# Kernel optimization log

Hardware: AMD Instinct MI355X
Metric: run time of the kernel (lower is better)

The kernel has to match this reference:

```python
import jax, jax.numpy as jnp
import numpy as np

N = 50000
IN_CH = 128
HID = 256
HEADS = 8
HEAD_DIM = HID // HEADS
NUM_CLASSES = 2
E = 800000
NEG_SLOPE = 0.2  # PyG GATConv default leaky_relu slope


def gat_conv(x, edge_index, W, att_src, att_dst, bias):
    """PyG-style GATConv (concat=True, add_self_loops=True, eval mode).
    x: [N, HID]; edge_index: [2, E] (row 0 = source j, row 1 = target i).
    W: [HID, HEADS*HEAD_DIM]; att_src/att_dst: [HEADS, HEAD_DIM]; bias: [HEADS*HEAD_DIM].
    """
    loop = jnp.arange(N)
    src = jnp.concatenate([edge_index[0], loop])  # self-loops appended
    dst = jnp.concatenate([edge_index[1], loop])
    h = (x @ W).reshape(N, HEADS, HEAD_DIM)          # [N, H, D]
    a_src = jnp.einsum('nhd,hd->nh', h, att_src)     # [N, H]
    a_dst = jnp.einsum('nhd,hd->nh', h, att_dst)
    e = jax.nn.leaky_relu(a_src[src] + a_dst[dst], NEG_SLOPE)  # [E+N, H]
    # segment softmax over incoming edges of each target node
    m = jax.ops.segment_max(e, dst, num_segments=N)
    p = jnp.exp(e - m[dst])
    s = jax.ops.segment_sum(p, dst, num_segments=N)
    alpha = p / (s[dst] + 1e-16)                     # [E+N, H]
    msg = h[src] * alpha[:, :, None]                 # [E+N, H, D]
    out = jax.ops.segment_sum(msg, dst, num_segments=N)  # [N, H, D]
    return out.reshape(N, HEADS * HEAD_DIM) + bias


def setup_inputs() -> dict:
    key = jax.random.key(0)
    ks = jax.random.split(key, 24)
    g = lambda k, shape, fan_in: jax.random.normal(k, shape, dtype=jnp.float32) / np.sqrt(fan_in)
    inp = {}
    inp['x'] = jax.random.normal(ks[0], (N, IN_CH), dtype=jnp.float32)
    inp['tut_edge_index'] = jax.random.randint(ks[1], (2, E), 0, N)
    inp['tdt_edge_index'] = jax.random.randint(ks[2], (2, E), 0, N)
    inp['proj_W'] = g(ks[3], (IN_CH, HID), IN_CH)
    inp['proj_b'] = jnp.zeros((HID,), jnp.float32)
    # 2 GAT layers per meta-path, stacked on leading axis
    inp['tut_W'] = g(ks[4], (2, HID, HID), HID)
    inp['tut_asrc'] = g(ks[5], (2, HEADS, HEAD_DIM), HEAD_DIM)
    inp['tut_adst'] = g(ks[6], (2, HEADS, HEAD_DIM), HEAD_DIM)
    inp['tut_bias'] = jnp.zeros((2, HID), jnp.float32)
    inp['tdt_W'] = g(ks[7], (2, HID, HID), HID)
    inp['tdt_asrc'] = g(ks[8], (2, HEADS, HEAD_DIM), HEAD_DIM)
    inp['tdt_adst'] = g(ks[9], (2, HEADS, HEAD_DIM), HEAD_DIM)
    inp['tdt_bias'] = jnp.zeros((2, HID), jnp.float32)
    inp['sem_att'] = jnp.full((2,), 0.5, jnp.float32)
    inp['cls_W1'] = g(ks[10], (HID, HID // 2), HID)
    inp['cls_b1'] = jnp.zeros((HID // 2,), jnp.float32)
    inp['cls_W2'] = g(ks[11], (HID // 2, NUM_CLASSES), HID // 2)
    inp['cls_b2'] = jnp.zeros((NUM_CLASSES,), jnp.float32)
    return inp


def reference(x, tut_edge_index, tdt_edge_index, proj_W, proj_b,
              tut_W, tut_asrc, tut_adst, tut_bias,
              tdt_W, tdt_asrc, tdt_adst, tdt_bias,
              sem_att, cls_W1, cls_b1, cls_W2, cls_b2):
    h = x @ proj_W + proj_b
    # TUT branch: 2 GATConv layers (eval mode -> dropout is identity)
    h_tut = h
    for l in range(2):
        h_tut = gat_conv(h_tut, tut_edge_index, tut_W[l], tut_asrc[l], tut_adst[l], tut_bias[l])
        h_tut = jax.nn.elu(h_tut)
    # TDT branch
    h_tdt = h
    for l in range(2):
        h_tdt = gat_conv(h_tdt, tdt_edge_index, tdt_W[l], tdt_asrc[l], tdt_adst[l], tdt_bias[l])
        h_tdt = jax.nn.elu(h_tdt)
    w = jax.nn.softmax(sem_att)
    z = w[0] * h_tut + w[1] * h_tdt
    hc = jax.nn.relu(z @ cls_W1 + cls_b1)
    logits = hc @ cls_W2 + cls_b2  # [N, NUM_CLASSES]
    return logits
```

## Files before the change

kernel.cpp:

```cpp
#include <hip/hip_runtime.h>
#include <hip/hip_fp16.h>
#include <cstddef>
#include <cstdint>


#define HID        256
#define HEADS      8
#define NEG_SLOPE  0.2f

#define BSH     7
#define BNODES  128
#define MAXNB   512
#define CH      2048

typedef __attribute__((ext_vector_type(8))) short short8v;
typedef __attribute__((ext_vector_type(4))) float float4v;

static __device__ __forceinline__ unsigned short f32_to_bf16(float v) {
    union { float f; unsigned u; } c; c.f = v;
    unsigned r = c.u + 0x7FFFu + ((c.u >> 16) & 1u);
    return (unsigned short)(r >> 16);
}
static __device__ __forceinline__ float bf16_to_f32(unsigned short b) {
    union { unsigned u; float f; } c; c.u = ((unsigned)b) << 16;
    return c.f;
}
static __device__ __forceinline__ void split_bf16(float v, unsigned short& hi, unsigned short& lo) {
    hi = f32_to_bf16(v);
    lo = f32_to_bf16(v - bf16_to_f32(hi));
}
static __device__ __forceinline__ void gload_lds16(const void* g, void* l) {
    __builtin_amdgcn_global_load_lds((const __attribute__((address_space(1))) void*)g,
                                     (__attribute__((address_space(3))) void*)l, 16, 0, 0);
}

template<int MODE>
__global__ __launch_bounds__(256) void mfma_gemm_kernel(
    const unsigned short* __restrict__ Ahi, const unsigned short* __restrict__ Alo,
    const unsigned short* __restrict__ Bthi, const unsigned short* __restrict__ Btlo,
    const float* __restrict__ bias,
    unsigned short* __restrict__ Chi, unsigned short* __restrict__ Clo,
    __half* __restrict__ Cf16, float* __restrict__ Cf32,
    int M, int N, int K)
{
    __shared__ __align__(16) short lds[4 * 4096];

    const int tid  = threadIdx.x;
    const int lane = tid & 63;
    const int w    = tid >> 6;
    const int wr   = w >> 1;
    const int wc   = w & 1;
    const int m0   = blockIdx.y * 128;
    const int n0   = blockIdx.x * 128;

    const unsigned short* sbase = (w == 0) ? Ahi : (w == 1) ? Alo : (w == 2) ? Bthi : Btlo;
    const int rowbase = (w < 2) ? m0 : n0;
    const int rowlim  = ((w < 2) ? M : N) - 1;

    float4v acc[4][4];
    #pragma unroll
    for (int i = 0; i < 4; ++i)
        #pragma unroll
        for (int j = 0; j < 4; ++j)
            acc[i][j] = (float4v){0.f, 0.f, 0.f, 0.f};

    const int kcl = lane >> 4;
    const int rl  = lane & 15;

    for (int k0 = 0; k0 < K; k0 += 32) {
        #pragma unroll
        for (int rh = 0; rh < 2; ++rh) {
            int row = rowbase + rh * 64 + lane;
            row = row > rowlim ? rowlim : row;
            const unsigned short* src = sbase + (size_t)row * K + k0;
            #pragma unroll
            for (int kc = 0; kc < 4; ++kc) {
                short* dst = &lds[w * 4096 + kc * 1024 + rh * 512];
                gload_lds16(src + kc * 8, dst);
            }
        }
        __syncthreads();

        short8v ahi[4], alo[4], bhi[4], blo[4];
        #pragma unroll
        for (int i = 0; i < 4; ++i) {
            int am = wr * 64 + i * 16 + rl;
            int bn = wc * 64 + i * 16 + rl;
            ahi[i] = *(const short8v*)&lds[0 * 4096 + kcl * 1024 + am * 8];
            alo[i] = *(const short8v*)&lds[1 * 4096 + kcl * 1024 + am * 8];
            bhi[i] = *(const short8v*)&lds[2 * 4096 + kcl * 1024 + bn * 8];
            blo[i] = *(const short8v*)&lds[3 * 4096 + kcl * 1024 + bn * 8];
        }
        #pragma unroll
        for (int i = 0; i < 4; ++i)
            #pragma unroll
            for (int j = 0; j < 4; ++j) {
                acc[i][j] = __builtin_amdgcn_mfma_f32_16x16x32_bf16(ahi[i], bhi[j], acc[i][j], 0, 0, 0);
                acc[i][j] = __builtin_amdgcn_mfma_f32_16x16x32_bf16(ahi[i], blo[j], acc[i][j], 0, 0, 0);
                acc[i][j] = __builtin_amdgcn_mfma_f32_16x16x32_bf16(alo[i], bhi[j], acc[i][j], 0, 0, 0);
            }
        __syncthreads();
    }

    const int cr = (lane >> 4) * 4;
    #pragma unroll
    for (int i = 0; i < 4; ++i) {
        #pragma unroll
        for (int r = 0; r < 4; ++r) {
            int row = m0 + wr * 64 + i * 16 + cr + r;
            if (row >= M) continue;
            #pragma unroll
            for (int j = 0; j < 4; ++j) {
                int col = n0 + wc * 64 + j * 16 + rl;
                float v = acc[i][j][r];
                if (bias) v += bias[col];
                if (MODE == 0) {
                    unsigned short h, l;
                    split_bf16(v, h, l);
                    Chi[(size_t)row * N + col] = h;
                    Clo[(size_t)row * N + col] = l;
                } else if (MODE == 1) {
                    Cf16[(size_t)row * N + col] = __float2half(v);
                } else {
                    Cf32[(size_t)row * N + col] = fmaxf(v, 0.f);
                }
            }
        }
    }
}

__global__ void prep_kernel(
    const float* __restrict__ proj_W, const float* __restrict__ tut_W,
    const float* __restrict__ tdt_W, const float* __restrict__ cls_W1,
    unsigned short* __restrict__ pWthi, unsigned short* __restrict__ pWtlo,
    unsigned short* __restrict__ tWthi, unsigned short* __restrict__ tWtlo,
    unsigned short* __restrict__ dWthi, unsigned short* __restrict__ dWtlo,
    unsigned short* __restrict__ cWthi, unsigned short* __restrict__ cWtlo,
    const float* __restrict__ x,
    unsigned short* __restrict__ xhi, unsigned short* __restrict__ xlo, int count4x)
{
    const int tid = blockIdx.x * blockDim.x + threadIdx.x;
    const int stride = gridDim.x * blockDim.x;
    for (int idx = tid; idx < 327680; idx += stride) {
        unsigned short h, l;
        if (idx < 32768) {
            int k = idx >> 8, n = idx & 255;
            split_bf16(proj_W[idx], h, l);
            pWthi[n * 128 + k] = h; pWtlo[n * 128 + k] = l;
        } else if (idx < 163840) {
            int r = idx - 32768;
            int ly = r >> 16, rr = r & 65535;
            int k = rr >> 8, n = rr & 255;
            split_bf16(tut_W[r], h, l);
            tWthi[ly * 65536 + n * 256 + k] = h; tWtlo[ly * 65536 + n * 256 + k] = l;
        } else if (idx < 294912) {
            int r = idx - 163840;
            int ly = r >> 16, rr = r & 65535;
            int k = rr >> 8, n = rr & 255;
            split_bf16(tdt_W[r], h, l);
            dWthi[ly * 65536 + n * 256 + k] = h; dWtlo[ly * 65536 + n * 256 + k] = l;
        } else {
            int r = idx - 294912;
            int k = r >> 7, n = r & 127;
            split_bf16(cls_W1[r], h, l);
            cWthi[n * 256 + k] = h; cWtlo[n * 256 + k] = l;
        }
    }
    for (int i = tid; i < count4x; i += stride) {
        float4 v = reinterpret_cast<const float4*>(x)[i];
        ushort4 hh, ll;
        split_bf16(v.x, hh.x, ll.x);
        split_bf16(v.y, hh.y, ll.y);
        split_bf16(v.z, hh.z, ll.z);
        split_bf16(v.w, hh.w, ll.w);
        reinterpret_cast<ushort4*>(xhi)[i] = hh;
        reinterpret_cast<ushort4*>(xlo)[i] = ll;
    }
}

__global__ __launch_bounds__(256) void att_kernel(
    const __half* __restrict__ hW,
    const float* __restrict__ att_src, const float* __restrict__ att_dst,
    float* __restrict__ a_src, float* __restrict__ a_dst, int n_nodes)
{
    const int wave = threadIdx.x >> 6;
    const int lane = threadIdx.x & 63;
    const int n = blockIdx.x * 4 + wave;
    if (n >= n_nodes) return;

    const __half2* hp = reinterpret_cast<const __half2*>(&hW[(size_t)n * HID + lane * 4]);
    __half2 h01 = hp[0], h23 = hp[1];
    float hx = __low2float(h01), hy = __high2float(h01);
    float hz = __low2float(h23), hw = __high2float(h23);
    float4 s4 = *reinterpret_cast<const float4*>(&att_src[lane * 4]);
    float4 d4 = *reinterpret_cast<const float4*>(&att_dst[lane * 4]);
    float ps = hx * s4.x + hy * s4.y + hz * s4.z + hw * s4.w;
    float pd = hx * d4.x + hy * d4.y + hz * d4.z + hw * d4.w;
    #pragma unroll
    for (int off = 1; off < 8; off <<= 1) {
        ps += __shfl_xor(ps, off);
        pd += __shfl_xor(pd, off);
    }
    if ((lane & 7) == 0) {
        a_src[n * HEADS + (lane >> 3)] = ps;
        a_dst[n * HEADS + (lane >> 3)] = pd;
    }
}

template<int OMODE>
__global__ __launch_bounds__(256) void gat_kernel(
    const __half* __restrict__ hW,
    const float* __restrict__ a_src, const float* __restrict__ a_dst,
    const int* __restrict__ row_ptr, const int* __restrict__ adj,
    const float* __restrict__ bias,
    const unsigned short* __restrict__ prevHi, const unsigned short* __restrict__ prevLo,
    const float* __restrict__ sem,
    unsigned short* __restrict__ outhi, unsigned short* __restrict__ outlo,
    int n_nodes)
{
    const int wave = threadIdx.x >> 6;
    const int lane = threadIdx.x & 63;
    const int n = blockIdx.x * 4 + wave;
    if (n >= n_nodes) return;

    const int beg = row_ptr[n];
    const int end = row_ptr[n + 1];
    const int h2 = lane >> 3;
    const int sl = lane & 7;
    const int hw = lane >> 5;
    const int l32 = lane & 31;
    const int d0 = l32 * 8;
    const int ah = (l32 >> 2) * 8;

    const float adst = a_dst[n * HEADS + h2];

    float m = -INFINITY, s = 0.f;
    float acc[8];
    #pragma unroll
    for (int k = 0; k < 8; ++k) acc[k] = 0.f;

    for (int j = beg; j < end; j += 8) {
        const int js = j + sl;
        const int valid = js < end;
        int src_l = valid ? adj[js] : 0;
        float e = -INFINITY;
        if (valid) {
            e = a_src[src_l * HEADS + h2] + adst;
            e = (e > 0.f) ? e : NEG_SLOPE * e;
        }
        float me = e;
        me = fmaxf(me, __shfl_xor(me, 1));
        me = fmaxf(me, __shfl_xor(me, 2));
        me = fmaxf(me, __shfl_xor(me, 4));
        const float m_new = fmaxf(m, me);
        const float p = __expf(e - m_new);
        float ps = p;
        ps += __shfl_xor(ps, 1);
        ps += __shfl_xor(ps, 2);
        ps += __shfl_xor(ps, 4);
        if (__any(m_new > m)) {
            const float scale = __expf(m - m_new);
            const float scale_g = __shfl(scale, ah);
            s *= scale;
            #pragma unroll
            for (int k = 0; k < 8; ++k) acc[k] *= scale_g;
            m = m_new;
        }
        s += ps;

        #pragma unroll
        for (int it = 0; it < 4; ++it) {
            const int jj = it * 2 + hw;
            const float alpha = __shfl(p, ah | jj);
            const int srce = __shfl(src_l, jj);
            if (j + jj < end) {
                float4 raw = *reinterpret_cast<const float4*>(&hW[(size_t)srce * HID + d0]);
                __half2 v0 = *reinterpret_cast<__half2*>(&raw.x);
                __half2 v1 = *reinterpret_cast<__half2*>(&raw.y);
                __half2 v2 = *reinterpret_cast<__half2*>(&raw.z);
                __half2 v3 = *reinterpret_cast<__half2*>(&raw.w);
                acc[0] += alpha * __low2float(v0); acc[1] += alpha * __high2float(v0);
                acc[2] += alpha * __low2float(v1); acc[3] += alpha * __high2float(v1);
                acc[4] += alpha * __low2float(v2); acc[5] += alpha * __high2float(v2);
                acc[6] += alpha * __low2float(v3); acc[7] += alpha * __high2float(v3);
            }
        }
    }

    #pragma unroll
    for (int k = 0; k < 8; ++k) acc[k] += __shfl_xor(acc[k], 32);

    const float inv = 1.f / (s + 1e-16f);
    const float inv_g = __shfl(inv, ah);

    if (lane < 32) {
        float4 b0 = *reinterpret_cast<const float4*>(&bias[d0]);
        float4 b1 = *reinterpret_cast<const float4*>(&bias[d0 + 4]);
        float o[8];
        o[0] = acc[0] * inv_g + b0.x; o[1] = acc[1] * inv_g + b0.y;
        o[2] = acc[2] * inv_g + b0.z; o[3] = acc[3] * inv_g + b0.w;
        o[4] = acc[4] * inv_g + b1.x; o[5] = acc[5] * inv_g + b1.y;
        o[6] = acc[6] * inv_g + b1.z; o[7] = acc[7] * inv_g + b1.w;
        #pragma unroll
        for (int k = 0; k < 8; ++k)
            o[k] = (o[k] > 0.f) ? o[k] : expm1f(o[k]);

        if (OMODE == 1) {
            const float e0 = __expf(sem[0]);
            const float e1 = __expf(sem[1]);
            const float w0 = e0 / (e0 + e1);
            const float w1 = e1 / (e0 + e1);
            ushort4 ph0 = *reinterpret_cast<const ushort4*>(&prevHi[(size_t)n * HID + d0]);
            ushort4 ph1 = *reinterpret_cast<const ushort4*>(&prevHi[(size_t)n * HID + d0 + 4]);
            ushort4 pl0 = *reinterpret_cast<const ushort4*>(&prevLo[(size_t)n * HID + d0]);
            ushort4 pl1 = *reinterpret_cast<const ushort4*>(&prevLo[(size_t)n * HID + d0 + 4]);
            o[0] = w0 * (bf16_to_f32(ph0.x) + bf16_to_f32(pl0.x)) + w1 * o[0];
            o[1] = w0 * (bf16_to_f32(ph0.y) + bf16_to_f32(pl0.y)) + w1 * o[1];
            o[2] = w0 * (bf16_to_f32(ph0.z) + bf16_to_f32(pl0.z)) + w1 * o[2];
            o[3] = w0 * (bf16_to_f32(ph0.w) + bf16_to_f32(pl0.w)) + w1 * o[3];
            o[4] = w0 * (bf16_to_f32(ph1.x) + bf16_to_f32(pl1.x)) + w1 * o[4];
            o[5] = w0 * (bf16_to_f32(ph1.y) + bf16_to_f32(pl1.y)) + w1 * o[5];
            o[6] = w0 * (bf16_to_f32(ph1.z) + bf16_to_f32(pl1.z)) + w1 * o[6];
            o[7] = w0 * (bf16_to_f32(ph1.w) + bf16_to_f32(pl1.w)) + w1 * o[7];
        }

        ushort4 oh0, oh1, ol0, ol1;
        split_bf16(o[0], oh0.x, ol0.x); split_bf16(o[1], oh0.y, ol0.y);
        split_bf16(o[2], oh0.z, ol0.z); split_bf16(o[3], oh0.w, ol0.w);
        split_bf16(o[4], oh1.x, ol1.x); split_bf16(o[5], oh1.y, ol1.y);
        split_bf16(o[6], oh1.z, ol1.z); split_bf16(o[7], oh1.w, ol1.w);
        *reinterpret_cast<ushort4*>(&outhi[(size_t)n * HID + d0])     = oh0;
        *reinterpret_cast<ushort4*>(&outhi[(size_t)n * HID + d0 + 4]) = oh1;
        *reinterpret_cast<ushort4*>(&outlo[(size_t)n * HID + d0])     = ol0;
        *reinterpret_cast<ushort4*>(&outlo[(size_t)n * HID + d0 + 4]) = ol1;
    }
}

__global__ __launch_bounds__(256) void bucket_count_kernel(
    const int* __restrict__ tut_dst, const int* __restrict__ tdt_dst,
    int* __restrict__ gcount, int E, int NB)
{
    __shared__ int hist[MAXNB];
    const int g = blockIdx.y;
    const int* dstp = g ? tdt_dst : tut_dst;
    for (int i = threadIdx.x; i < MAXNB; i += 256) hist[i] = 0;
    __syncthreads();
    for (int e = blockIdx.x * 256 + threadIdx.x; e < E; e += gridDim.x * 256)
        atomicAdd(&hist[dstp[e] >> BSH], 1);
    __syncthreads();
    for (int i = threadIdx.x; i < NB; i += 256) {
        int c = hist[i];
        if (c) atomicAdd(&gcount[g * NB + i], c);
    }
}

__global__ __launch_bounds__(512) void bucket_scan_kernel(
    const int* __restrict__ gcount, int* __restrict__ ebase, int* __restrict__ adjbase,
    int* __restrict__ rp0, int* __restrict__ rp1, int N, int E, int NB)
{
    __shared__ int sa[MAXNB], sb[MAXNB];
    const int t = threadIdx.x;
    for (int g = 0; g < 2; ++g) {
        int cnt = (t < NB) ? gcount[g * NB + t] : 0;
        int nodes = 0;
        if (t < NB) { int s = t << BSH; nodes = (N - s < BNODES) ? (N - s) : BNODES; }
        sa[t] = cnt;
        sb[t] = cnt + nodes;
        __syncthreads();
        for (int off = 1; off < MAXNB; off <<= 1) {
            int va = (t >= off) ? sa[t - off] : 0;
            int vb = (t >= off) ? sb[t - off] : 0;
            __syncthreads();
            sa[t] += va; sb[t] += vb;
            __syncthreads();
        }
        if (t < NB) {
            ebase[g * (NB + 1) + t + 1] = sa[t];
            adjbase[g * (NB + 1) + t + 1] = sb[t];
        }
        if (t == 0) { ebase[g * (NB + 1)] = 0; adjbase[g * (NB + 1)] = 0; }
        __syncthreads();
    }
    if (t == 0) { rp0[N] = E + N; rp1[N] = E + N; }
}

__global__ __launch_bounds__(256) void bucket_bin_kernel(
    const int* __restrict__ tut_ei, const int* __restrict__ tdt_ei,
    const int* __restrict__ ebase, int* __restrict__ gcursor,
    int2* __restrict__ ebuf, int E, int NB)
{
    __shared__ int lhist[MAXNB];
    __shared__ int lbase[MAXNB];
    __shared__ int loffs[MAXNB];
    __shared__ int2 spair[CH];
    __shared__ int saddr[CH];
    const int g = blockIdx.y;
    const int* ei = g ? tdt_ei : tut_ei;
    const int e0 = blockIdx.x * CH;
    const int cnt = (E - e0 < CH) ? (E - e0) : CH;

    for (int i = threadIdx.x; i < MAXNB; i += 256) lhist[i] = 0;
    __syncthreads();

    int myb[8], myrank[8], mysrc[8], mydst[8];
    int nmine = 0;
    #pragma unroll
    for (int k = 0; k < 8; ++k) {
        int idx = e0 + threadIdx.x + k * 256;
        if (idx < e0 + cnt) {
            int sv = ei[idx];
            int dv = ei[E + idx];
            int b = dv >> BSH;
            int r = atomicAdd(&lhist[b], 1);
            myb[nmine] = b; myrank[nmine] = r; mysrc[nmine] = sv; mydst[nmine] = dv;
            ++nmine;
        }
    }
    __syncthreads();
    loffs[threadIdx.x] = lhist[threadIdx.x];
    loffs[threadIdx.x + 256] = lhist[threadIdx.x + 256];
    __syncthreads();
    for (int off = 1; off < MAXNB; off <<= 1) {
        int i0 = threadIdx.x, i1 = threadIdx.x + 256;
        int v0 = (i0 >= off) ? loffs[i0 - off] : 0;
        int v1 = (i1 >= off) ? loffs[i1 - off] : 0;
        __syncthreads();
        loffs[i0] += v0; loffs[i1] += v1;
        __syncthreads();
    }
    for (int i = threadIdx.x; i < NB; i += 256) {
        int c = lhist[i];
        lbase[i] = c ? atomicAdd(&gcursor[g * NB + i], c) : 0;
    }
    __syncthreads();
    const int* eb = ebase + g * (NB + 1);
    for (int k = 0; k < nmine; ++k) {
        int b = myb[k];
        int sorted = loffs[b] - lhist[b] + myrank[k];
        spair[sorted] = make_int2(mysrc[k], mydst[k]);
        saddr[sorted] = eb[b] + lbase[b] + myrank[k];
    }
    __syncthreads();
    int2* out = ebuf + (size_t)g * E;
    for (int i = threadIdx.x; i < cnt; i += 256)
        out[saddr[i]] = spair[i];
}

__global__ __launch_bounds__(256) void bucket_csr_kernel(
    const int* __restrict__ gcount, const int* __restrict__ ebase,
    const int* __restrict__ adjbase, const int2* __restrict__ ebuf,
    int* __restrict__ rp0, int* __restrict__ rp1,
    int* __restrict__ adj0, int* __restrict__ adj1, int N, int E, int NB)
{
    __shared__ int hist[BNODES], scn[BNODES], cursor[BNODES];
    const int g = blockIdx.y;
    const int b = blockIdx.x;
    int* rp  = g ? rp1 : rp0;
    int* adj = g ? adj1 : adj0;
    const int cnt = gcount[g * NB + b];
    const int aB  = adjbase[g * (NB + 1) + b];
    const int node0 = b << BSH;
    const int nb = (N - node0 < BNODES) ? (N - node0) : BNODES;
    const int2* ep = ebuf + (size_t)g * E + ebase[g * (NB + 1) + b];
    const int t = threadIdx.x;

    if (t < BNODES) hist[t] = 0;
    __syncthreads();
    for (int e = t; e < cnt; e += 256)
        atomicAdd(&hist[ep[e].y - node0], 1);
    __syncthreads();
    if (t < BNODES) scn[t] = (t < nb) ? hist[t] + 1 : 0;
    __syncthreads();
    for (int off = 1; off < BNODES; off <<= 1) {
        int v = 0;
        if (t < BNODES && t >= off) v = scn[t - off];
        __syncthreads();
        if (t < BNODES) scn[t] += v;
        __syncthreads();
    }
    if (t < nb) {
        int s = scn[t] - hist[t] - 1;
        rp[node0 + t] = aB + s;
        adj[aB + s] = node0 + t;
        cursor[t] = s + 1;
    }
    __syncthreads();
    for (int e = t; e < cnt; e += 256) {
        int2 pr = ep[e];
        int pos = atomicAdd(&cursor[pr.y - node0], 1);
        adj[aB + pos] = pr.x;
    }
}

__global__ __launch_bounds__(256) void cls2_kernel(
    const float* __restrict__ hc, const float* __restrict__ W2,
    const float* __restrict__ b2, float* __restrict__ out, int n_nodes)
{
    const int wave = threadIdx.x >> 6;
    const int lane = threadIdx.x & 63;
    const int n = blockIdx.x * 4 + wave;
    if (n >= n_nodes) return;
    float h0 = hc[(size_t)n * 128 + lane];
    float h1 = hc[(size_t)n * 128 + 64 + lane];
    float p0 = h0 * W2[lane * 2 + 0] + h1 * W2[(64 + lane) * 2 + 0];
    float p1 = h0 * W2[lane * 2 + 1] + h1 * W2[(64 + lane) * 2 + 1];
    #pragma unroll
    for (int off = 1; off < 64; off <<= 1) {
        p0 += __shfl_xor(p0, off);
        p1 += __shfl_xor(p1, off);
    }
    if (lane == 0) {
        out[(size_t)n * 2 + 0] = p0 + b2[0];
        out[(size_t)n * 2 + 1] = p1 + b2[1];
    }
}

extern "C" void kernel_launch(void* const* d_in, const int* in_sizes, int n_in,
                              void* d_out, int out_size, void* d_ws, size_t ws_size,
                              hipStream_t stream)
{
    const float* x        = (const float*)d_in[0];
    const int*   tut_ei   = (const int*)d_in[1];
    const int*   tdt_ei   = (const int*)d_in[2];
    const float* proj_W   = (const float*)d_in[3];
    const float* proj_b   = (const float*)d_in[4];
    const float* tut_W    = (const float*)d_in[5];
    const float* tut_asrc = (const float*)d_in[6];
    const float* tut_adst = (const float*)d_in[7];
    const float* tut_bias = (const float*)d_in[8];
    const float* tdt_W    = (const float*)d_in[9];
    const float* tdt_asrc = (const float*)d_in[10];
    const float* tdt_adst = (const float*)d_in[11];
    const float* tdt_bias = (const float*)d_in[12];
    const float* sem_att  = (const float*)d_in[13];
    const float* cls_W1   = (const float*)d_in[14];
    const float* cls_b1   = (const float*)d_in[15];
    const float* cls_W2   = (const float*)d_in[16];
    const float* cls_b2   = (const float*)d_in[17];

    const int IN_CH = 128;
    const int N = in_sizes[0] / IN_CH;
    const int E = in_sizes[1] / 2;
    const int NB = (N + BNODES - 1) >> BSH;
    const size_t NH = (size_t)N * HID;
    const size_t NI = (size_t)N * IN_CH;

    char* base = (char*)d_ws;
    size_t off = 0;
    auto alloc = [&](size_t bytes) -> void* {
        void* p = base + off;
        off = (off + bytes + 255) & ~(size_t)255;
        return p;
    };
    unsigned short* xhi  = (unsigned short*)alloc(NI * 2);
    unsigned short* xlo  = (unsigned short*)alloc(NI * 2);
    unsigned short* t2lo = (unsigned short*)alloc(NH * 2);
    unsigned short* h0hi = (unsigned short*)alloc(NH * 2);
    unsigned short* h0lo = (unsigned short*)alloc(NH * 2);
    unsigned short* l1hi = (unsigned short*)alloc(NH * 2);
    unsigned short* l1lo = (unsigned short*)alloc(NH * 2);
    __half*         hWf  = (__half*)alloc(NH * 2);
    float* a_src = (float*)alloc((size_t)N * HEADS * sizeof(float));
    float* a_dst = (float*)alloc((size_t)N * HEADS * sizeof(float));
    unsigned short* pWthi = (unsigned short*)alloc(256 * 128 * 2);
    unsigned short* pWtlo = (unsigned short*)alloc(256 * 128 * 2);
    unsigned short* tWthi = (unsigned short*)alloc(2 * 256 * 256 * 2);
    unsigned short* tWtlo = (unsigned short*)alloc(2 * 256 * 256 * 2);
    unsigned short* dWthi = (unsigned short*)alloc(2 * 256 * 256 * 2);
    unsigned short* dWtlo = (unsigned short*)alloc(2 * 256 * 256 * 2);
    unsigned short* cWthi = (unsigned short*)alloc(128 * 256 * 2);
    unsigned short* cWtlo = (unsigned short*)alloc(128 * 256 * 2);
    int* rp_tut  = (int*)alloc((size_t)(N + 1) * sizeof(int));
    int* adj_tut = (int*)alloc((size_t)(E + N) * sizeof(int));
    int* rp_tdt  = (int*)alloc((size_t)(N + 1) * sizeof(int));
    int* adj_tdt = (int*)alloc((size_t)(E + N) * sizeof(int));
    int* gbuf    = (int*)alloc((size_t)4 * NB * sizeof(int));
    int* gcount  = gbuf;
    int* gcursor = gbuf + 2 * NB;
    int* ebase   = (int*)alloc((size_t)2 * (NB + 1) * sizeof(int));
    int* adjbase = (int*)alloc((size_t)2 * (NB + 1) * sizeof(int));
    (void)ws_size; (void)n_in; (void)out_size;

    int2* ebuf = (int2*)hWf;
    unsigned short* t2hi = xhi;
    unsigned short* zhi  = l1hi;
    unsigned short* zlo  = l1lo;
    float*          hc   = (float*)hWf;

    const int nodeBlocks = (N + 3) / 4;

    hipMemsetAsync(gbuf, 0, (size_t)4 * NB * sizeof(int), stream);
    prep_kernel<<<1024, 256, 0, stream>>>(proj_W, tut_W, tdt_W, cls_W1,
                                          pWthi, pWtlo, tWthi, tWtlo, dWthi, dWtlo,
                                          cWthi, cWtlo, x, xhi, xlo, (int)(NI / 4));
    bucket_count_kernel<<<dim3(128, 2), 256, 0, stream>>>(tut_ei + E, tdt_ei + E, gcount, E, NB);
    bucket_scan_kernel<<<1, 512, 0, stream>>>(gcount, ebase, adjbase, rp_tut, rp_tdt, N, E, NB);
    bucket_bin_kernel<<<dim3((E + CH - 1) / CH, 2), 256, 0, stream>>>(
        tut_ei, tdt_ei, ebase, gcursor, ebuf, E, NB);
    bucket_csr_kernel<<<dim3(NB, 2), 256, 0, stream>>>(
        gcount, ebase, adjbase, ebuf, rp_tut, rp_tdt, adj_tut, adj_tdt, N, E, NB);

    const int gy = (N + 127) / 128;

    mfma_gemm_kernel<0><<<dim3(2, gy), 256, 0, stream>>>(
        xhi, xlo, pWthi, pWtlo, proj_b, h0hi, h0lo, nullptr, nullptr, N, HID, IN_CH);

    auto run_gemm_att = [&](const unsigned short* ahi, const unsigned short* alo,
                            const unsigned short* wthi, const unsigned short* wtlo,
                            const float* asrc_w, const float* adst_w) {
        mfma_gemm_kernel<1><<<dim3(2, gy), 256, 0, stream>>>(
            ahi, alo, wthi, wtlo, nullptr, nullptr, nullptr, hWf, nullptr, N, HID, HID);
        att_kernel<<<nodeBlocks, 256, 0, stream>>>(hWf, asrc_w, adst_w, a_src, a_dst, N);
    };

    const int WT = 256 * 256;
    const int AS = HEADS * (HID / HEADS);

    run_gemm_att(h0hi, h0lo, tWthi, tWtlo, tut_asrc, tut_adst);
    gat_kernel<0><<<nodeBlocks, 256, 0, stream>>>(
        hWf, a_src, a_dst, rp_tut, adj_tut, tut_bias,
        nullptr, nullptr, nullptr, l1hi, l1lo, N);
    run_gemm_att(l1hi, l1lo, tWthi + WT, tWtlo + WT, tut_asrc + AS, tut_adst + AS);
    gat_kernel<0><<<nodeBlocks, 256, 0, stream>>>(
        hWf, a_src, a_dst, rp_tut, adj_tut, tut_bias + HID,
        nullptr, nullptr, nullptr, t2hi, t2lo, N);
    run_gemm_att(h0hi, h0lo, dWthi, dWtlo, tdt_asrc, tdt_adst);
    gat_kernel<0><<<nodeBlocks, 256, 0, stream>>>(
        hWf, a_src, a_dst, rp_tdt, adj_tdt, tdt_bias,
        nullptr, nullptr, nullptr, l1hi, l1lo, N);
    run_gemm_att(l1hi, l1lo, dWthi + WT, dWtlo + WT, tdt_asrc + AS, tdt_adst + AS);
    gat_kernel<1><<<nodeBlocks, 256, 0, stream>>>(
        hWf, a_src, a_dst, rp_tdt, adj_tdt, tdt_bias + HID,
        t2hi, t2lo, sem_att, zhi, zlo, N);

    mfma_gemm_kernel<2><<<dim3(1, gy), 256, 0, stream>>>(
        zhi, zlo, cWthi, cWtlo, cls_b1, nullptr, nullptr, nullptr, hc, N, 128, HID);
    cls2_kernel<<<nodeBlocks, 256, 0, stream>>>(hc, cls_W2, cls_b2, (float*)d_out, N);
}
```

Measured before the change: 738.2 us.

## Split GAT aggregation into a softmax-stats pass and a normalized gather pass

Replaces the single-pass online softmax with two passes. The first pass computes each head's max and sum per node with per-lane online accumulation followed by a cross-lane merge. The second pass recomputes each edge's attention logit and multiplies by the final normalized alpha while gathering features. This removes the per-chunk shuffles, the wave-wide rescale checks and the accumulator rescaling, at the cost of reading the adjacency and a_src twice and recomputing exp per edge.

```diff
diff --git a/kernel.cpp b/kernel.cpp
--- a/kernel.cpp
+++ b/kernel.cpp
@@ -225,56 +225,54 @@
 
     const int beg = row_ptr[n];
     const int end = row_ptr[n + 1];
-    const int h2 = lane >> 3;
-    const int sl = lane & 7;
+    const int h1 = lane & 7;
+    const int sl = lane >> 3;
     const int hw = lane >> 5;
     const int l32 = lane & 31;
     const int d0 = l32 * 8;
-    const int ah = (l32 >> 2) * 8;
-
-    const float adst = a_dst[n * HEADS + h2];
+    const int hd = l32 >> 2;
+
+    const float adst1 = a_dst[n * HEADS + h1];
 
     float m = -INFINITY, s = 0.f;
+    for (int j = beg + sl; j < end; j += 8) {
+        float e = a_src[adj[j] * HEADS + h1] + adst1;
+        e = (e > 0.f) ? e : NEG_SLOPE * e;
+        float mn = fmaxf(m, e);
+        float t = (m > -INFINITY) ? s * __expf(m - mn) : 0.f;
+        s = t + __expf(e - mn);
+        m = mn;
+    }
+    #pragma unroll
+    for (int off = 8; off < 64; off <<= 1) {
+        float mo = __shfl_xor(m, off);
+        float so = __shfl_xor(s, off);
+        float mn = fmaxf(m, mo);
+        float t1 = (m  > -INFINITY) ? s  * __expf(m  - mn) : 0.f;
+        float t2 = (mo > -INFINITY) ? so * __expf(mo - mn) : 0.f;
+        s = t1 + t2;
+        m = mn;
+    }
+
+    const float mh    = __shfl(m, hd);
+    const float sh    = __shfl(s, hd);
+    const float adst2 = __shfl(adst1, hd);
+    const float inv   = 1.f / (sh + 1e-16f);
+
     float acc[8];
     #pragma unroll
     for (int k = 0; k < 8; ++k) acc[k] = 0.f;
 
     for (int j = beg; j < end; j += 8) {
-        const int js = j + sl;
-        const int valid = js < end;
-        int src_l = valid ? adj[js] : 0;
-        float e = -INFINITY;
-        if (valid) {
-            e = a_src[src_l * HEADS + h2] + adst;
-            e = (e > 0.f) ? e : NEG_SLOPE * e;
-        }
-        float me = e;
-        me = fmaxf(me, __shfl_xor(me, 1));
-        me = fmaxf(me, __shfl_xor(me, 2));
-        me = fmaxf(me, __shfl_xor(me, 4));
-        const float m_new = fmaxf(m, me);
-        const float p = __expf(e - m_new);
-        float ps = p;
-        ps += __shfl_xor(ps, 1);
-        ps += __shfl_xor(ps, 2);
-        ps += __shfl_xor(ps, 4);
-        if (__any(m_new > m)) {
-            const float scale = __expf(m - m_new);
-            const float scale_g = __shfl(scale, ah);
-            s *= scale;
-            #pragma unroll
-            for (int k = 0; k < 8; ++k) acc[k] *= scale_g;
-            m = m_new;
-        }
-        s += ps;
-
         #pragma unroll
         for (int it = 0; it < 4; ++it) {
-            const int jj = it * 2 + hw;
-            const float alpha = __shfl(p, ah | jj);
-            const int srce = __shfl(src_l, jj);
-            if (j + jj < end) {
-                float4 raw = *reinterpret_cast<const float4*>(&hW[(size_t)srce * HID + d0]);
+            const int jj = j + it * 2 + hw;
+            if (jj < end) {
+                const int src = adj[jj];
+                float e = a_src[src * HEADS + hd] + adst2;
+                e = (e > 0.f) ? e : NEG_SLOPE * e;
+                const float alpha = __expf(e - mh) * inv;
+                float4 raw = *reinterpret_cast<const float4*>(&hW[(size_t)src * HID + d0]);
                 __half2 v0 = *reinterpret_cast<__half2*>(&raw.x);
                 __half2 v1 = *reinterpret_cast<__half2*>(&raw.y);
                 __half2 v2 = *reinterpret_cast<__half2*>(&raw.z);
@@ -290,17 +288,14 @@
     #pragma unroll
     for (int k = 0; k < 8; ++k) acc[k] += __shfl_xor(acc[k], 32);
 
-    const float inv = 1.f / (s + 1e-16f);
-    const float inv_g = __shfl(inv, ah);
-
     if (lane < 32) {
         float4 b0 = *reinterpret_cast<const float4*>(&bias[d0]);
         float4 b1 = *reinterpret_cast<const float4*>(&bias[d0 + 4]);
         float o[8];
-        o[0] = acc[0] * inv_g + b0.x; o[1] = acc[1] * inv_g + b0.y;
-        o[2] = acc[2] * inv_g + b0.z; o[3] = acc[3] * inv_g + b0.w;
-        o[4] = acc[4] * inv_g + b1.x; o[5] = acc[5] * inv_g + b1.y;
-        o[6] = acc[6] * inv_g + b1.z; o[7] = acc[7] * inv_g + b1.w;
+        o[0] = acc[0] + b0.x; o[1] = acc[1] + b0.y;
+        o[2] = acc[2] + b0.z; o[3] = acc[3] + b0.w;
+        o[4] = acc[4] + b1.x; o[5] = acc[5] + b1.y;
+        o[6] = acc[6] + b1.z; o[7] = acc[7] + b1.w;
         #pragma unroll
         for (int k = 0; k < 8; ++k)
             o[k] = (o[k] > 0.f) ? o[k] : expm1f(o[k]);
```

New measurement: 777.6 us. 5.3% more time.
